# Optimization experiments

Measured on AMD Instinct MI355X. Metric: run time of the kernel, lower is better.

The kernel has to match this reference:

```python
import jax, jax.numpy as jnp
import numpy as np

E, B, C, M, H = 8, 2, 1024, 2048, 7168


def setup_inputs() -> dict:
    key = jax.random.key(0)
    k1, k2, k3, k4 = jax.random.split(key, 4)
    # kaiming_uniform-ish scale for weights (bound = sqrt(6/fan_in)/sqrt(1+5) ~ 1/sqrt(fan_in))
    s_in = 1.0 / np.sqrt(M)
    s_ffn = 1.0 / np.sqrt(H)
    return {
        "dispatch_input": jax.random.normal(k1, (E, B, C, M), dtype=jnp.float32),
        "w1": jax.random.uniform(k2, (E, M, H), dtype=jnp.float32, minval=-s_in, maxval=s_in),
        "w2": jax.random.uniform(k3, (E, H, M), dtype=jnp.float32, minval=-s_ffn, maxval=s_ffn),
        "w3": jax.random.uniform(k4, (E, M, H), dtype=jnp.float32, minval=-s_in, maxval=s_in),
    }


def reference(dispatch_input, w1, w2, w3):
    # Batched per-expert SwiGLU MLP.
    # gate: [E,B,C,H], up: [E,B,C,H]
    gate = jnp.einsum("ebcm,emh->ebch", dispatch_input, w1)
    up = jnp.einsum("ebcm,emh->ebch", dispatch_input, w3)
    hidden = jax.nn.silu(gate) * up
    out = jnp.einsum("ebch,ehm->ebcm", hidden, w2)
    return out
```

## Files before the change

### kernel.cpp

```cpp
#include <hip/hip_runtime.h>

typedef __attribute__((ext_vector_type(8))) short bf16x8;
typedef __attribute__((ext_vector_type(4))) float f32x4;
typedef __attribute__((ext_vector_type(4))) unsigned int u32x4;
typedef __attribute__((ext_vector_type(4))) unsigned short u16x4;

#define NE 8
#define NT 2048
#define NM 2048
#define NH 7168

#define BAR() asm volatile("s_barrier" ::: "memory")
#define WAITV(N) asm volatile("s_waitcnt vmcnt(" #N ")" ::: "memory")

__device__ __forceinline__ unsigned short f2bf(float f) {
    unsigned int u = __float_as_uint(f);
    return (unsigned short)((u + 0x7fffu + ((u >> 16) & 1u)) >> 16);
}

__device__ __forceinline__ void gld16(const void* g, void* l) {
    __builtin_amdgcn_global_load_lds(
        (const __attribute__((address_space(1))) void*)g,
        (__attribute__((address_space(3))) void*)l, 16, 0, 0);
}


__global__ __launch_bounds__(256) void convert_x_kernel(
        const float* __restrict__ in, unsigned short* __restrict__ out) {
    const int i = blockIdx.x * 256 + threadIdx.x;
    f32x4 a = ((const f32x4*)in)[i];
    ((u16x4*)out)[i] = (u16x4){f2bf(a[0]), f2bf(a[1]), f2bf(a[2]), f2bf(a[3])};
}

__global__ __launch_bounds__(256) void convert_wT_kernel(
        const float* __restrict__ in, unsigned short* __restrict__ out,
        int R, int C) {
    const int t = threadIdx.x;
    const int e = blockIdx.y;
    const int tiles_c = C >> 6;
    const int tr = blockIdx.x / tiles_c, tc = blockIdx.x % tiles_c;

    const float* ip = in + (size_t)e * R * C + (size_t)(tr * 64) * C + tc * 64;
    unsigned short* op = out + (size_t)e * R * C + (size_t)(tc * 64) * R + tr * 64;

    __shared__ unsigned short tl[64][68];

    const int rr = t >> 4, c4 = (t & 15) * 4;
#pragma unroll
    for (int q = 0; q < 4; ++q) {
        const int r = q * 16 + rr;
        f32x4 v = *(const f32x4*)(ip + (size_t)r * C + c4);
        *(u16x4*)&tl[r][c4] = (u16x4){f2bf(v[0]), f2bf(v[1]), f2bf(v[2]), f2bf(v[3])};
    }
    __syncthreads();
#pragma unroll
    for (int q = 0; q < 4; ++q) {
        const int oc = q * 16 + rr;
        u16x4 v = (u16x4){tl[c4][oc], tl[c4 + 1][oc], tl[c4 + 2][oc], tl[c4 + 3][oc]};
        *(u16x4*)(op + (size_t)oc * R + c4) = v;
    }
}

__global__ __launch_bounds__(256) void convert_w13_kernel(
        const float* __restrict__ w1, const float* __restrict__ w3,
        unsigned short* __restrict__ wcat) {
    const int t = threadIdx.x;
    const int e = blockIdx.y;
    const int tiles_c = NH >> 6;
    const int tr = blockIdx.x / tiles_c, tc = blockIdx.x % tiles_c;

    __shared__ unsigned short tl[64][68];
    const int rr = t >> 4, c4 = (t & 15) * 4;
    unsigned short* ob = wcat + (size_t)e * (2 * NH) * NM + (size_t)(tc * 128) * NM + tr * 64;

#pragma unroll
    for (int pass = 0; pass < 2; ++pass) {
        const float* ip = (pass ? w3 : w1) + (size_t)e * NM * NH + (size_t)(tr * 64) * NH + tc * 64;
        if (pass) __syncthreads();
#pragma unroll
        for (int q = 0; q < 4; ++q) {
            const int r = q * 16 + rr;
            f32x4 v = *(const f32x4*)(ip + (size_t)r * NH + c4);
            *(u16x4*)&tl[r][c4] = (u16x4){f2bf(v[0]), f2bf(v[1]), f2bf(v[2]), f2bf(v[3])};
        }
        __syncthreads();
#pragma unroll
        for (int q = 0; q < 4; ++q) {
            const int oc = q * 16 + rr;
            const int orow = ((oc >> 4) * 32) + pass * 16 + (oc & 15);
            u16x4 v = (u16x4){tl[c4][oc], tl[c4 + 1][oc], tl[c4 + 2][oc], tl[c4 + 3][oc]};
            *(u16x4*)(ob + (size_t)orow * NM + c4) = v;
        }
    }
}

__global__ __launch_bounds__(512, 2) void gemm1p_kernel(
        const unsigned short* __restrict__ xb, const unsigned short* __restrict__ wcat,
        unsigned short* __restrict__ hid) {
    const int tid = threadIdx.x;
    const int lane = tid & 63, wv = tid >> 6;
    const int wr = wv >> 2, wc = wv & 3;
    const int e = blockIdx.y;
    const int d = blockIdx.x;
    const int l = (d & 7) * 56 + (d >> 3);
    const int ct = l >> 3, tt = l & 7;

    const unsigned short* ag = xb   + (size_t)(e * NT + tt * 256) * NM;
    const unsigned short* bg = wcat + (size_t)e * (2 * NH) * NM + (size_t)(ct * 256) * NM;
    unsigned short* hg = hid + (size_t)(e * NT + tt * 256) * NH + ct * 128;

    __shared__ __align__(16) unsigned short lds[3 * 16384];

    const int frow = lane & 15;
    const int fks  = (lane >> 4) * 8;
    const int la   = lane * 8;
    const int lr   = lane & 15, lq = lane >> 4;

    f32x4 acc[8][4];
#pragma unroll
    for (int m = 0; m < 8; ++m)
#pragma unroll
        for (int n = 0; n < 4; ++n) acc[m][n] = (f32x4){0.f, 0.f, 0.f, 0.f};

    auto stageA = [&](int t, int buf) {
        unsigned short* dst = lds + buf * 16384 + wv * 512;
        const unsigned short* src = ag + (size_t)(wv * 16 + frow) * NM + t * 32 + fks;
        gld16(src, dst);
        gld16(src + (size_t)128 * NM, dst + 8 * 512);
    };
    auto stageB = [&](int t, int buf) {
        unsigned short* dst = lds + buf * 16384 + 8192 + wv * 512;
        const unsigned short* src = bg + (size_t)(wv * 16 + frow) * NM + t * 32 + fks;
        gld16(src, dst);
        gld16(src + (size_t)128 * NM, dst + 8 * 512);
    };

    auto body = [&](int t, int buf, bool st2, int nbuf) {
        const unsigned short* bA = lds + buf * 16384;
        const unsigned short* bB = bA + 8192;
        bf16x8 af[4], bf[4];
        BAR();
#pragma unroll
        for (int m = 0; m < 4; ++m)
            af[m] = *(const bf16x8*)(bA + (wr * 8 + m) * 512 + la);
#pragma unroll
        for (int n = 0; n < 4; ++n)
            bf[n] = *(const bf16x8*)(bB + (wc * 4 + n) * 512 + la);
        __builtin_amdgcn_s_setprio(1);
#pragma unroll
        for (int m = 0; m < 4; ++m)
#pragma unroll
            for (int n = 0; n < 4; ++n)
                acc[m][n] = __builtin_amdgcn_mfma_f32_16x16x32_bf16(af[m], bf[n], acc[m][n], 0, 0, 0);
        __builtin_amdgcn_s_setprio(0);
        if (st2) stageB(t + 2, nbuf);
#pragma unroll
        for (int m = 0; m < 4; ++m)
            af[m] = *(const bf16x8*)(bA + (wr * 8 + 4 + m) * 512 + la);
        __builtin_amdgcn_s_setprio(1);
#pragma unroll
        for (int m = 0; m < 4; ++m)
#pragma unroll
            for (int n = 0; n < 4; ++n)
                acc[4 + m][n] = __builtin_amdgcn_mfma_f32_16x16x32_bf16(af[m], bf[n], acc[4 + m][n], 0, 0, 0);
        __builtin_amdgcn_s_setprio(0);
        BAR();
    };

    const int NKT = NM / 32;
    stageA(0, 0); stageB(0, 0);
    stageA(1, 1); stageB(1, 1);

    int buf = 0, nbuf = 2;
    for (int t = 0; t < NKT - 2; ++t) {
        stageA(t + 2, nbuf);
        WAITV(6);
        body(t, buf, true, nbuf);
        buf = (buf == 2) ? 0 : buf + 1;
        nbuf = (nbuf == 2) ? 0 : nbuf + 1;
    }
    WAITV(4);
    body(NKT - 2, buf, false, 0);
    buf = (buf == 2) ? 0 : buf + 1;
    WAITV(0);
    body(NKT - 1, buf, false, 0);

#pragma unroll
    for (int mf = 0; mf < 8; ++mf)
#pragma unroll
        for (int p = 0; p < 2; ++p)
#pragma unroll
            for (int i = 0; i < 4; ++i) {
                const float g = acc[mf][2 * p][i];
                const float u = acc[mf][2 * p + 1][i];
                const float s = g / (1.f + __expf(-g));
                const int r = wr * 128 + mf * 16 + lq * 4 + i;
                const int h = wc * 32 + p * 16 + lr;
                hg[(size_t)r * NH + h] = f2bf(s * u);
            }
}

__global__ __launch_bounds__(512, 2) void gemm2p_kernel(
        const unsigned short* __restrict__ hid, const unsigned short* __restrict__ w2t,
        float* __restrict__ out) {
    const int tid = threadIdx.x;
    const int lane = tid & 63, wv = tid >> 6;
    const int wr = wv >> 2, wc = wv & 3;
    const int e = blockIdx.y;
    const int d = blockIdx.x;
    const int l = (d & 7) * 8 + (d >> 3);
    const int mt = l >> 3, tt = l & 7;

    const unsigned short* ag = hid + (size_t)(e * NT + tt * 256) * NH;
    const unsigned short* bg = w2t + (size_t)e * NM * NH + (size_t)(mt * 256) * NH;
    float* og = out + (size_t)(e * NT + tt * 256) * NM + mt * 256;

    __shared__ __align__(16) unsigned short lds[3 * 16384];

    const int frow = lane & 15;
    const int fks  = (lane >> 4) * 8;
    const int la   = lane * 8;
    const int lr   = lane & 15, lq = lane >> 4;

    f32x4 acc[8][4];
#pragma unroll
    for (int m = 0; m < 8; ++m)
#pragma unroll
        for (int n = 0; n < 4; ++n) acc[m][n] = (f32x4){0.f, 0.f, 0.f, 0.f};

    auto stageA = [&](int t, int buf) {
        unsigned short* dst = lds + buf * 16384 + wv * 512;
        const unsigned short* src = ag + (size_t)(wv * 16 + frow) * NH + t * 32 + fks;
        gld16(src, dst);
        gld16(src + (size_t)128 * NH, dst + 8 * 512);
    };
    auto stageB = [&](int t, int buf) {
        unsigned short* dst = lds + buf * 16384 + 8192 + wv * 512;
        const unsigned short* src = bg + (size_t)(wv * 16 + frow) * NH + t * 32 + fks;
        gld16(src, dst);
        gld16(src + (size_t)128 * NH, dst + 8 * 512);
    };

    auto body = [&](int t, int buf, bool st2, int nbuf) {
        const unsigned short* bA = lds + buf * 16384;
        const unsigned short* bB = bA + 8192;
        bf16x8 af[4], bf[4];
        BAR();
#pragma unroll
        for (int m = 0; m < 4; ++m)
            af[m] = *(const bf16x8*)(bA + (wr * 8 + m) * 512 + la);
#pragma unroll
        for (int n = 0; n < 4; ++n)
            bf[n] = *(const bf16x8*)(bB + (wc * 4 + n) * 512 + la);
        __builtin_amdgcn_s_setprio(1);
#pragma unroll
        for (int m = 0; m < 4; ++m)
#pragma unroll
            for (int n = 0; n < 4; ++n)
                acc[m][n] = __builtin_amdgcn_mfma_f32_16x16x32_bf16(af[m], bf[n], acc[m][n], 0, 0, 0);
        __builtin_amdgcn_s_setprio(0);
        if (st2) stageB(t + 2, nbuf);
#pragma unroll
        for (int m = 0; m < 4; ++m)
            af[m] = *(const bf16x8*)(bA + (wr * 8 + 4 + m) * 512 + la);
        __builtin_amdgcn_s_setprio(1);
#pragma unroll
        for (int m = 0; m < 4; ++m)
#pragma unroll
            for (int n = 0; n < 4; ++n)
                acc[4 + m][n] = __builtin_amdgcn_mfma_f32_16x16x32_bf16(af[m], bf[n], acc[4 + m][n], 0, 0, 0);
        __builtin_amdgcn_s_setprio(0);
        BAR();
    };

    const int NKT = NH / 32;
    stageA(0, 0); stageB(0, 0);
    stageA(1, 1); stageB(1, 1);

    int buf = 0, nbuf = 2;
    for (int t = 0; t < NKT - 2; ++t) {
        stageA(t + 2, nbuf);
        WAITV(6);
        body(t, buf, true, nbuf);
        buf = (buf == 2) ? 0 : buf + 1;
        nbuf = (nbuf == 2) ? 0 : nbuf + 1;
    }
    WAITV(4);
    body(NKT - 2, buf, false, 0);
    buf = (buf == 2) ? 0 : buf + 1;
    WAITV(0);
    body(NKT - 1, buf, false, 0);

#pragma unroll
    for (int mf = 0; mf < 8; ++mf)
#pragma unroll
        for (int n = 0; n < 4; ++n)
#pragma unroll
            for (int i = 0; i < 4; ++i) {
                const int r = wr * 128 + mf * 16 + lq * 4 + i;
                const int c = wc * 64 + n * 16 + lr;
                og[(size_t)r * NM + c] = acc[mf][n][i];
            }
}

#define ROWB 80
#define TILEB (128 * ROWB)

__global__ __launch_bounds__(256, 2) void gemm1_fb_kernel(
        const float* __restrict__ x, const float* __restrict__ w1,
        const float* __restrict__ w3, unsigned short* __restrict__ hid) {
    const int tid = threadIdx.x;
    const int e = blockIdx.y;
    const int d = blockIdx.x;
    const int l = (d & 7) * 112 + (d >> 3);
    const int hn = l >> 4, tm = l & 15;

    const float* xg  = x  + (size_t)(e * NT + tm * 128) * NM;
    const float* w1g = w1 + (size_t)e * NM * NH + hn * 128;
    const float* w3g = w3 + (size_t)e * NM * NH + hn * 128;
    unsigned short* hg = hid + (size_t)(e * NT + tm * 128) * NH + hn * 128;

    __shared__ __align__(16) unsigned char lds[2 * 3 * TILEB];

    const int a_r = tid >> 3, a_c4 = tid & 7;
    const int w_kq = (tid >> 2) & 7;
    const int w_cg = ((tid >> 5) << 2) | (tid & 3);

    const int lane = tid & 63;
    const int wv = tid >> 6;
    const int r0w = (wv >> 1) * 64, c0w = (wv & 1) * 64;
    const int lr = lane & 15, lq = lane >> 4;

    f32x4 accg[4][4], accu[4][4];
#pragma unroll
    for (int m = 0; m < 4; ++m)
#pragma unroll
        for (int n = 0; n < 4; ++n) {
            accg[m][n] = (f32x4){0.f, 0.f, 0.f, 0.f};
            accu[m][n] = (f32x4){0.f, 0.f, 0.f, 0.f};
        }

    f32x4 la0, la1, la2, la3;
    f32x4 l10, l11, l12, l13, l30, l31, l32, l33;

    auto stage_load = [&](int ks) {
        const int k0 = ks * 32;
        const float* pa = xg + (size_t)a_r * NM + k0 + a_c4 * 4;
        la0 = *(const f32x4*)(pa);
        la1 = *(const f32x4*)(pa + 32 * NM);
        la2 = *(const f32x4*)(pa + 64 * NM);
        la3 = *(const f32x4*)(pa + 96 * NM);
        const float* p1 = w1g + (size_t)(k0 + w_kq * 4) * NH + w_cg * 4;
        l10 = *(const f32x4*)(p1);
        l11 = *(const f32x4*)(p1 + NH);
        l12 = *(const f32x4*)(p1 + 2 * NH);
        l13 = *(const f32x4*)(p1 + 3 * NH);
        const float* p3 = w3g + (size_t)(k0 + w_kq * 4) * NH + w_cg * 4;
        l30 = *(const f32x4*)(p3);
        l31 = *(const f32x4*)(p3 + NH);
        l32 = *(const f32x4*)(p3 + 2 * NH);
        l33 = *(const f32x4*)(p3 + 3 * NH);
    };

    auto stage_write = [&](int buf) {
        unsigned char* base = lds + buf * (3 * TILEB);
        unsigned char* pa = base + a_r * ROWB + a_c4 * 8;
        *(u16x4*)(pa)             = (u16x4){f2bf(la0[0]), f2bf(la0[1]), f2bf(la0[2]), f2bf(la0[3])};
        *(u16x4*)(pa + 32 * ROWB) = (u16x4){f2bf(la1[0]), f2bf(la1[1]), f2bf(la1[2]), f2bf(la1[3])};
        *(u16x4*)(pa + 64 * ROWB) = (u16x4){f2bf(la2[0]), f2bf(la2[1]), f2bf(la2[2]), f2bf(la2[3])};
        *(u16x4*)(pa + 96 * ROWB) = (u16x4){f2bf(la3[0]), f2bf(la3[1]), f2bf(la3[2]), f2bf(la3[3])};
        unsigned char* pw1 = base + TILEB + w_kq * 8;
#pragma unroll
        for (int j = 0; j < 4; ++j) {
            const int c = w_cg * 4 + j;
            *(u16x4*)(pw1 + c * ROWB) =
                (u16x4){f2bf(l10[j]), f2bf(l11[j]), f2bf(l12[j]), f2bf(l13[j])};
        }
        unsigned char* pw3 = base + 2 * TILEB + w_kq * 8;
#pragma unroll
        for (int j = 0; j < 4; ++j) {
            const int c = w_cg * 4 + j;
            *(u16x4*)(pw3 + c * ROWB) =
                (u16x4){f2bf(l30[j]), f2bf(l31[j]), f2bf(l32[j]), f2bf(l33[j])};
        }
    };

    auto compute = [&](int buf) {
        const unsigned char* base = lds + buf * (3 * TILEB);
        bf16x8 af[4], b1f[4], b3f[4];
#pragma unroll
        for (int m = 0; m < 4; ++m)
            af[m] = *(const bf16x8*)(base + (r0w + m * 16 + lr) * ROWB + lq * 16);
#pragma unroll
        for (int n = 0; n < 4; ++n) {
            b1f[n] = *(const bf16x8*)(base + TILEB + (c0w + n * 16 + lr) * ROWB + lq * 16);
            b3f[n] = *(const bf16x8*)(base + 2 * TILEB + (c0w + n * 16 + lr) * ROWB + lq * 16);
        }
#pragma unroll
        for (int m = 0; m < 4; ++m)
#pragma unroll
            for (int n = 0; n < 4; ++n) {
                accg[m][n] = __builtin_amdgcn_mfma_f32_16x16x32_bf16(af[m], b1f[n], accg[m][n], 0, 0, 0);
                accu[m][n] = __builtin_amdgcn_mfma_f32_16x16x32_bf16(af[m], b3f[n], accu[m][n], 0, 0, 0);
            }
    };

    stage_load(0);
    stage_write(0);
    __syncthreads();
    int cur = 0;
    const int NK = NM / 32;
    for (int ks = 0; ks < NK; ++ks) {
        const bool more = (ks + 1 < NK);
        if (more) stage_load(ks + 1);
        compute(cur);
        if (more) {
            stage_write(cur ^ 1);
            __syncthreads();
        }
        cur ^= 1;
    }

#pragma unroll
    for (int m = 0; m < 4; ++m)
#pragma unroll
        for (int n = 0; n < 4; ++n)
#pragma unroll
            for (int i = 0; i < 4; ++i) {
                const float g = accg[m][n][i];
                const float u = accu[m][n][i];
                const float s = g / (1.f + __expf(-g));
                const int r = r0w + m * 16 + lq * 4 + i;
                const int c = c0w + n * 16 + lr;
                hg[(size_t)r * NH + c] = f2bf(s * u);
            }
}

__global__ __launch_bounds__(256, 2) void gemm2_fb_kernel(
        const unsigned short* __restrict__ hid, const float* __restrict__ w2,
        float* __restrict__ out) {
    const int tid = threadIdx.x;
    const int e = blockIdx.y;
    const int d = blockIdx.x;
    const int l = (d & 7) * 32 + (d >> 3);
    const int mn = l >> 4, tm = l & 15;

    const unsigned short* ag = hid + (size_t)(e * NT + tm * 128) * NH;
    const float* wg = w2 + (size_t)e * NH * NM + mn * 128;
    float* og = out + (size_t)(e * NT + tm * 128) * NM + mn * 128;

    __shared__ __align__(16) unsigned char lds[2 * 2 * TILEB];

    const int a_row = tid >> 2, a_ch = tid & 3;
    const int w_kq = (tid >> 2) & 7;
    const int w_cg = ((tid >> 5) << 2) | (tid & 3);

    const int lane = tid & 63;
    const int wv = tid >> 6;
    const int r0w = (wv >> 1) * 64, c0w = (wv & 1) * 64;
    const int lr = lane & 15, lq = lane >> 4;

    f32x4 acc[4][4];
#pragma unroll
    for (int m = 0; m < 4; ++m)
#pragma unroll
        for (int n = 0; n < 4; ++n) acc[m][n] = (f32x4){0.f, 0.f, 0.f, 0.f};

    u32x4 lau0, lau1;
    f32x4 lw0, lw1, lw2, lw3;

    auto stage_load = [&](int ks) {
        const int k0 = ks * 32;
        lau0 = *(const u32x4*)(ag + (size_t)a_row * NH + k0 + a_ch * 8);
        lau1 = *(const u32x4*)(ag + (size_t)(a_row + 64) * NH + k0 + a_ch * 8);
        const float* p = wg + (size_t)(k0 + w_kq * 4) * NM + w_cg * 4;
        lw0 = *(const f32x4*)(p);
        lw1 = *(const f32x4*)(p + NM);
        lw2 = *(const f32x4*)(p + 2 * NM);
        lw3 = *(const f32x4*)(p + 3 * NM);
    };

    auto stage_write = [&](int buf) {
        unsigned char* base = lds + buf * (2 * TILEB);
        *(u32x4*)(base + a_row * ROWB + a_ch * 16) = lau0;
        *(u32x4*)(base + (a_row + 64) * ROWB + a_ch * 16) = lau1;
        unsigned char* pw = base + TILEB + w_kq * 8;
#pragma unroll
        for (int j = 0; j < 4; ++j) {
            const int c = w_cg * 4 + j;
            *(u16x4*)(pw + c * ROWB) =
                (u16x4){f2bf(lw0[j]), f2bf(lw1[j]), f2bf(lw2[j]), f2bf(lw3[j])};
        }
    };

    auto compute = [&](int buf) {
        const unsigned char* base = lds + buf * (2 * TILEB);
        bf16x8 af[4], bf[4];
#pragma unroll
        for (int m = 0; m < 4; ++m)
            af[m] = *(const bf16x8*)(base + (r0w + m * 16 + lr) * ROWB + lq * 16);
#pragma unroll
        for (int n = 0; n < 4; ++n)
            bf[n] = *(const bf16x8*)(base + TILEB + (c0w + n * 16 + lr) * ROWB + lq * 16);
#pragma unroll
        for (int m = 0; m < 4; ++m)
#pragma unroll
            for (int n = 0; n < 4; ++n)
                acc[m][n] = __builtin_amdgcn_mfma_f32_16x16x32_bf16(af[m], bf[n], acc[m][n], 0, 0, 0);
    };

    stage_load(0);
    stage_write(0);
    __syncthreads();
    int cur = 0;
    const int NK = NH / 32;
    for (int ks = 0; ks < NK; ++ks) {
        const bool more = (ks + 1 < NK);
        if (more) stage_load(ks + 1);
        compute(cur);
        if (more) {
            stage_write(cur ^ 1);
            __syncthreads();
        }
        cur ^= 1;
    }

#pragma unroll
    for (int m = 0; m < 4; ++m)
#pragma unroll
        for (int n = 0; n < 4; ++n)
#pragma unroll
            for (int i = 0; i < 4; ++i) {
                const int r = r0w + m * 16 + lq * 4 + i;
                const int c = c0w + n * 16 + lr;
                og[(size_t)r * NM + c] = acc[m][n][i];
            }
}


extern "C" void kernel_launch(void* const* d_in, const int* in_sizes, int n_in,
                              void* d_out, int out_size, void* d_ws, size_t ws_size,
                              hipStream_t stream) {
    const float* x  = (const float*)d_in[0];
    const float* w1 = (const float*)d_in[1];
    const float* w2 = (const float*)d_in[2];
    const float* w3 = (const float*)d_in[3];
    float* out = (float*)d_out;

    const size_t XB_SZ   = (size_t)NE * NT * NM * 2;
    const size_t WCAT_SZ = (size_t)NE * 2 * NH * NM * 2;
    const size_t HID_SZ  = (size_t)NE * NT * NH * 2;
    const size_t NEED = XB_SZ + WCAT_SZ + HID_SZ;

    if (ws_size >= NEED) {
        unsigned char* ws = (unsigned char*)d_ws;
        unsigned short* xbp  = (unsigned short*)(ws);
        unsigned short* wcat = (unsigned short*)(ws + XB_SZ);
        unsigned short* hidb = (unsigned short*)(ws + XB_SZ + WCAT_SZ);
        unsigned short* w2t  = (unsigned short*)(ws);

        convert_x_kernel<<<dim3((NE * NT * NM) / 1024), 256, 0, stream>>>(x, xbp);
        convert_w13_kernel<<<dim3((NM / 64) * (NH / 64), NE), 256, 0, stream>>>(w1, w3, wcat);
        gemm1p_kernel<<<dim3(448, NE), 512, 0, stream>>>(xbp, wcat, hidb);
        convert_wT_kernel<<<dim3((NH / 64) * (NM / 64), NE), 256, 0, stream>>>(w2, w2t, NH, NM);
        gemm2p_kernel<<<dim3(64, NE), 512, 0, stream>>>(hidb, w2t, out);
    } else {
        unsigned short* hid = (unsigned short*)d_ws;
        gemm1_fb_kernel<<<dim3(896, NE), 256, 0, stream>>>(x, w1, w3, hid);
        gemm2_fb_kernel<<<dim3(256, NE), 256, 0, stream>>>(hid, w2, out);
    }
}
```

Before: 1.937 ms.

## Load B fragments directly from global into registers, drop B LDS staging

Both bf16 GEMM kernels stop staging the B (weight) tile through LDS. Each wave now loads its B fragments straight from global memory into registers, double-buffered across two register sets, while A keeps its triple-buffered LDS pipeline. LDS use is halved and the B ds_reads go away. In exchange B loads lose sharing across the waves in a block (wr=0/1 waves fetch the same B), which raises global/L2 traffic. It also depends on hand-tuned vmcnt waits staying correct.

```diff
diff --git a/kernel.cpp b/kernel.cpp
--- a/kernel.cpp
+++ b/kernel.cpp
@@ -109,7 +109,7 @@
     const unsigned short* bg = wcat + (size_t)e * (2 * NH) * NM + (size_t)(ct * 256) * NM;
     unsigned short* hg = hid + (size_t)(e * NT + tt * 256) * NH + ct * 128;
 
-    __shared__ __align__(16) unsigned short lds[3 * 16384];
+    __shared__ __align__(16) unsigned short lds[3 * 8192];
 
     const int frow = lane & 15;
     const int fks  = (lane >> 4) * 8;
@@ -123,29 +123,23 @@
         for (int n = 0; n < 4; ++n) acc[m][n] = (f32x4){0.f, 0.f, 0.f, 0.f};
 
     auto stageA = [&](int t, int buf) {
-        unsigned short* dst = lds + buf * 16384 + wv * 512;
+        unsigned short* dst = lds + buf * 8192 + wv * 512;
         const unsigned short* src = ag + (size_t)(wv * 16 + frow) * NM + t * 32 + fks;
         gld16(src, dst);
         gld16(src + (size_t)128 * NM, dst + 8 * 512);
     };
-    auto stageB = [&](int t, int buf) {
-        unsigned short* dst = lds + buf * 16384 + 8192 + wv * 512;
-        const unsigned short* src = bg + (size_t)(wv * 16 + frow) * NM + t * 32 + fks;
-        gld16(src, dst);
-        gld16(src + (size_t)128 * NM, dst + 8 * 512);
-    };
-
-    auto body = [&](int t, int buf, bool st2, int nbuf) {
-        const unsigned short* bA = lds + buf * 16384;
-        const unsigned short* bB = bA + 8192;
-        bf16x8 af[4], bf[4];
-        BAR();
+    auto bload = [&](bf16x8 (&bf)[4], int t) {
+#pragma unroll
+        for (int n = 0; n < 4; ++n)
+            bf[n] = *(const bf16x8*)(bg + (size_t)(wc * 64 + n * 16 + lr) * NM + t * 32 + fks);
+    };
+
+    auto body = [&](int buf, const bf16x8 (&bf)[4]) {
+        const unsigned short* bA = lds + buf * 8192;
+        bf16x8 af[4];
 #pragma unroll
         for (int m = 0; m < 4; ++m)
             af[m] = *(const bf16x8*)(bA + (wr * 8 + m) * 512 + la);
-#pragma unroll
-        for (int n = 0; n < 4; ++n)
-            bf[n] = *(const bf16x8*)(bB + (wc * 4 + n) * 512 + la);
         __builtin_amdgcn_s_setprio(1);
 #pragma unroll
         for (int m = 0; m < 4; ++m)
@@ -153,7 +147,6 @@
             for (int n = 0; n < 4; ++n)
                 acc[m][n] = __builtin_amdgcn_mfma_f32_16x16x32_bf16(af[m], bf[n], acc[m][n], 0, 0, 0);
         __builtin_amdgcn_s_setprio(0);
-        if (st2) stageB(t + 2, nbuf);
 #pragma unroll
         for (int m = 0; m < 4; ++m)
             af[m] = *(const bf16x8*)(bA + (wr * 8 + 4 + m) * 512 + la);
@@ -164,26 +157,40 @@
             for (int n = 0; n < 4; ++n)
                 acc[4 + m][n] = __builtin_amdgcn_mfma_f32_16x16x32_bf16(af[m], bf[n], acc[4 + m][n], 0, 0, 0);
         __builtin_amdgcn_s_setprio(0);
+    };
+
+    const int NKT = NM / 32;
+    bf16x8 bfA[4], bfB[4];
+
+    stageA(0, 0);
+    bload(bfA, 0);
+    stageA(1, 1);
+
+    int buf = 0, nbuf = 2;
+    for (int t = 0; t < NKT - 2; t += 2) {
+        bload(bfB, t + 1);
+        stageA(t + 2, nbuf);
+        WAITV(12); BAR(); WAITV(8);
+        body(buf, bfA);
         BAR();
-    };
-
-    const int NKT = NM / 32;
-    stageA(0, 0); stageB(0, 0);
-    stageA(1, 1); stageB(1, 1);
-
-    int buf = 0, nbuf = 2;
-    for (int t = 0; t < NKT - 2; ++t) {
-        stageA(t + 2, nbuf);
-        WAITV(6);
-        body(t, buf, true, nbuf);
         buf = (buf == 2) ? 0 : buf + 1;
         nbuf = (nbuf == 2) ? 0 : nbuf + 1;
-    }
-    WAITV(4);
-    body(NKT - 2, buf, false, 0);
+
+        bload(bfA, t + 2);
+        stageA(t + 3, nbuf);
+        WAITV(12); BAR(); WAITV(8);
+        body(buf, bfB);
+        BAR();
+        buf = (buf == 2) ? 0 : buf + 1;
+        nbuf = (nbuf == 2) ? 0 : nbuf + 1;
+    }
+    bload(bfB, NKT - 1);
+    WAITV(10); BAR(); WAITV(6);
+    body(buf, bfA);
+    BAR();
     buf = (buf == 2) ? 0 : buf + 1;
-    WAITV(0);
-    body(NKT - 1, buf, false, 0);
+    WAITV(4); BAR(); WAITV(0);
+    body(buf, bfB);
 
 #pragma unroll
     for (int mf = 0; mf < 8; ++mf)
@@ -215,7 +222,7 @@
     const unsigned short* bg = w2t + (size_t)e * NM * NH + (size_t)(mt * 256) * NH;
     float* og = out + (size_t)(e * NT + tt * 256) * NM + mt * 256;
 
-    __shared__ __align__(16) unsigned short lds[3 * 16384];
+    __shared__ __align__(16) unsigned short lds[3 * 8192];
 
     const int frow = lane & 15;
     const int fks  = (lane >> 4) * 8;
@@ -229,29 +236,23 @@
         for (int n = 0; n < 4; ++n) acc[m][n] = (f32x4){0.f, 0.f, 0.f, 0.f};
 
     auto stageA = [&](int t, int buf) {
-        unsigned short* dst = lds + buf * 16384 + wv * 512;
+        unsigned short* dst = lds + buf * 8192 + wv * 512;
         const unsigned short* src = ag + (size_t)(wv * 16 + frow) * NH + t * 32 + fks;
         gld16(src, dst);
         gld16(src + (size_t)128 * NH, dst + 8 * 512);
     };
-    auto stageB = [&](int t, int buf) {
-        unsigned short* dst = lds + buf * 16384 + 8192 + wv * 512;
-        const unsigned short* src = bg + (size_t)(wv * 16 + frow) * NH + t * 32 + fks;
-        gld16(src, dst);
-        gld16(src + (size_t)128 * NH, dst + 8 * 512);
-    };
-
-    auto body = [&](int t, int buf, bool st2, int nbuf) {
-        const unsigned short* bA = lds + buf * 16384;
-        const unsigned short* bB = bA + 8192;
-        bf16x8 af[4], bf[4];
-        BAR();
+    auto bload = [&](bf16x8 (&bf)[4], int t) {
+#pragma unroll
+        for (int n = 0; n < 4; ++n)
+            bf[n] = *(const bf16x8*)(bg + (size_t)(wc * 64 + n * 16 + lr) * NH + t * 32 + fks);
+    };
+
+    auto body = [&](int buf, const bf16x8 (&bf)[4]) {
+        const unsigned short* bA = lds + buf * 8192;
+        bf16x8 af[4];
 #pragma unroll
         for (int m = 0; m < 4; ++m)
             af[m] = *(const bf16x8*)(bA + (wr * 8 + m) * 512 + la);
-#pragma unroll
-        for (int n = 0; n < 4; ++n)
-            bf[n] = *(const bf16x8*)(bB + (wc * 4 + n) * 512 + la);
         __builtin_amdgcn_s_setprio(1);
 #pragma unroll
         for (int m = 0; m < 4; ++m)
@@ -259,7 +260,6 @@
             for (int n = 0; n < 4; ++n)
                 acc[m][n] = __builtin_amdgcn_mfma_f32_16x16x32_bf16(af[m], bf[n], acc[m][n], 0, 0, 0);
         __builtin_amdgcn_s_setprio(0);
-        if (st2) stageB(t + 2, nbuf);
 #pragma unroll
         for (int m = 0; m < 4; ++m)
             af[m] = *(const bf16x8*)(bA + (wr * 8 + 4 + m) * 512 + la);
@@ -270,26 +270,40 @@
             for (int n = 0; n < 4; ++n)
                 acc[4 + m][n] = __builtin_amdgcn_mfma_f32_16x16x32_bf16(af[m], bf[n], acc[4 + m][n], 0, 0, 0);
         __builtin_amdgcn_s_setprio(0);
+    };
+
+    const int NKT = NH / 32;
+    bf16x8 bfA[4], bfB[4];
+
+    stageA(0, 0);
+    bload(bfA, 0);
+    stageA(1, 1);
+
+    int buf = 0, nbuf = 2;
+    for (int t = 0; t < NKT - 2; t += 2) {
+        bload(bfB, t + 1);
+        stageA(t + 2, nbuf);
+        WAITV(12); BAR(); WAITV(8);
+        body(buf, bfA);
         BAR();
-    };
-
-    const int NKT = NH / 32;
-    stageA(0, 0); stageB(0, 0);
-    stageA(1, 1); stageB(1, 1);
-
-    int buf = 0, nbuf = 2;
-    for (int t = 0; t < NKT - 2; ++t) {
-        stageA(t + 2, nbuf);
-        WAITV(6);
-        body(t, buf, true, nbuf);
         buf = (buf == 2) ? 0 : buf + 1;
         nbuf = (nbuf == 2) ? 0 : nbuf + 1;
-    }
-    WAITV(4);
-    body(NKT - 2, buf, false, 0);
+
+        bload(bfA, t + 2);
+        stageA(t + 3, nbuf);
+        WAITV(12); BAR(); WAITV(8);
+        body(buf, bfB);
+        BAR();
+        buf = (buf == 2) ? 0 : buf + 1;
+        nbuf = (nbuf == 2) ? 0 : nbuf + 1;
+    }
+    bload(bfB, NKT - 1);
+    WAITV(10); BAR(); WAITV(6);
+    body(buf, bfA);
+    BAR();
     buf = (buf == 2) ? 0 : buf + 1;
-    WAITV(0);
-    body(NKT - 1, buf, false, 0);
+    WAITV(4); BAR(); WAITV(0);
+    body(buf, bfB);
 
 #pragma unroll
     for (int mf = 0; mf < 8; ++mf)
```

Result: slower. 2.896 ms (+49.5%).

## Replace triple-buffered LDS pipeline with simple double buffering in both GEMMs

Applied to the files above, without the earlier changes.

Both bf16 GEMM kernels drop from a three-stage LDS ring with prefetch distance two, where the B load was interleaved mid-body, to two buffers with prefetch distance one. A and B for the next tile are issued together before the barrier. LDS use per block shrinks from 96KB to 64KB, which may ease occupancy pressure. The cost is less latency hiding for global loads and a simpler schedule that no longer splits the B stage between the MFMA halves.

```diff
diff --git a/kernel.cpp b/kernel.cpp
--- a/kernel.cpp
+++ b/kernel.cpp
@@ -109,7 +109,7 @@
     const unsigned short* bg = wcat + (size_t)e * (2 * NH) * NM + (size_t)(ct * 256) * NM;
     unsigned short* hg = hid + (size_t)(e * NT + tt * 256) * NH + ct * 128;
 
-    __shared__ __align__(16) unsigned short lds[3 * 16384];
+    __shared__ __align__(16) unsigned short lds[2 * 16384];
 
     const int frow = lane & 15;
     const int fks  = (lane >> 4) * 8;
@@ -135,11 +135,10 @@
         gld16(src + (size_t)128 * NM, dst + 8 * 512);
     };
 
-    auto body = [&](int t, int buf, bool st2, int nbuf) {
+    auto body = [&](int buf) {
         const unsigned short* bA = lds + buf * 16384;
         const unsigned short* bB = bA + 8192;
         bf16x8 af[4], bf[4];
-        BAR();
 #pragma unroll
         for (int m = 0; m < 4; ++m)
             af[m] = *(const bf16x8*)(bA + (wr * 8 + m) * 512 + la);
@@ -153,7 +152,6 @@
             for (int n = 0; n < 4; ++n)
                 acc[m][n] = __builtin_amdgcn_mfma_f32_16x16x32_bf16(af[m], bf[n], acc[m][n], 0, 0, 0);
         __builtin_amdgcn_s_setprio(0);
-        if (st2) stageB(t + 2, nbuf);
 #pragma unroll
         for (int m = 0; m < 4; ++m)
             af[m] = *(const bf16x8*)(bA + (wr * 8 + 4 + m) * 512 + la);
@@ -164,26 +162,25 @@
             for (int n = 0; n < 4; ++n)
                 acc[4 + m][n] = __builtin_amdgcn_mfma_f32_16x16x32_bf16(af[m], bf[n], acc[4 + m][n], 0, 0, 0);
         __builtin_amdgcn_s_setprio(0);
-        BAR();
     };
 
     const int NKT = NM / 32;
     stageA(0, 0); stageB(0, 0);
-    stageA(1, 1); stageB(1, 1);
-
-    int buf = 0, nbuf = 2;
-    for (int t = 0; t < NKT - 2; ++t) {
-        stageA(t + 2, nbuf);
-        WAITV(6);
-        body(t, buf, true, nbuf);
-        buf = (buf == 2) ? 0 : buf + 1;
-        nbuf = (nbuf == 2) ? 0 : nbuf + 1;
-    }
-    WAITV(4);
-    body(NKT - 2, buf, false, 0);
-    buf = (buf == 2) ? 0 : buf + 1;
-    WAITV(0);
-    body(NKT - 1, buf, false, 0);
+
+    int buf = 0;
+    for (int t = 0; t < NKT; ++t) {
+        if (t + 1 < NKT) {
+            stageA(t + 1, buf ^ 1);
+            stageB(t + 1, buf ^ 1);
+            WAITV(4);
+        } else {
+            WAITV(0);
+        }
+        BAR();
+        body(buf);
+        BAR();
+        buf ^= 1;
+    }
 
 #pragma unroll
     for (int mf = 0; mf < 8; ++mf)
@@ -215,7 +212,7 @@
     const unsigned short* bg = w2t + (size_t)e * NM * NH + (size_t)(mt * 256) * NH;
     float* og = out + (size_t)(e * NT + tt * 256) * NM + mt * 256;
 
-    __shared__ __align__(16) unsigned short lds[3 * 16384];
+    __shared__ __align__(16) unsigned short lds[2 * 16384];
 
     const int frow = lane & 15;
     const int fks  = (lane >> 4) * 8;
@@ -241,11 +238,10 @@
         gld16(src + (size_t)128 * NH, dst + 8 * 512);
     };
 
-    auto body = [&](int t, int buf, bool st2, int nbuf) {
+    auto body = [&](int buf) {
         const unsigned short* bA = lds + buf * 16384;
         const unsigned short* bB = bA + 8192;
         bf16x8 af[4], bf[4];
-        BAR();
 #pragma unroll
         for (int m = 0; m < 4; ++m)
             af[m] = *(const bf16x8*)(bA + (wr * 8 + m) * 512 + la);
@@ -259,7 +255,6 @@
             for (int n = 0; n < 4; ++n)
                 acc[m][n] = __builtin_amdgcn_mfma_f32_16x16x32_bf16(af[m], bf[n], acc[m][n], 0, 0, 0);
         __builtin_amdgcn_s_setprio(0);
-        if (st2) stageB(t + 2, nbuf);
 #pragma unroll
         for (int m = 0; m < 4; ++m)
             af[m] = *(const bf16x8*)(bA + (wr * 8 + 4 + m) * 512 + la);
@@ -270,26 +265,25 @@
             for (int n = 0; n < 4; ++n)
                 acc[4 + m][n] = __builtin_amdgcn_mfma_f32_16x16x32_bf16(af[m], bf[n], acc[4 + m][n], 0, 0, 0);
         __builtin_amdgcn_s_setprio(0);
-        BAR();
     };
 
     const int NKT = NH / 32;
     stageA(0, 0); stageB(0, 0);
-    stageA(1, 1); stageB(1, 1);
-
-    int buf = 0, nbuf = 2;
-    for (int t = 0; t < NKT - 2; ++t) {
-        stageA(t + 2, nbuf);
-        WAITV(6);
-        body(t, buf, true, nbuf);
-        buf = (buf == 2) ? 0 : buf + 1;
-        nbuf = (nbuf == 2) ? 0 : nbuf + 1;
-    }
-    WAITV(4);
-    body(NKT - 2, buf, false, 0);
-    buf = (buf == 2) ? 0 : buf + 1;
-    WAITV(0);
-    body(NKT - 1, buf, false, 0);
+
+    int buf = 0;
+    for (int t = 0; t < NKT; ++t) {
+        if (t + 1 < NKT) {
+            stageA(t + 1, buf ^ 1);
+            stageB(t + 1, buf ^ 1);
+            WAITV(4);
+        } else {
+            WAITV(0);
+        }
+        BAR();
+        body(buf);
+        BAR();
+        buf ^= 1;
+    }
 
 #pragma unroll
     for (int mf = 0; mf < 8; ++mf)
```

New measurement: 2.009 ms. 1.04x slower.

## Fold w2 transpose-convert into gemm1 launch as extra blocks

Applied to the files above, without the earlier changes.

Appends 1792 extra blocks to the gemm1 grid that perform the w2 fp32-to-bf16 transpose into a separate workspace region, removing the standalone convert_wT launch. The transpose work can then overlap with the tail of the first GEMM instead of running serially between the GEMMs. It needs extra workspace for w2t; if that is unavailable it falls back to the old path. Block scheduling order may delay GEMM blocks or compete for bandwidth.

```diff
diff --git a/kernel.cpp b/kernel.cpp
--- a/kernel.cpp
+++ b/kernel.cpp
@@ -96,20 +96,47 @@
 
 __global__ __launch_bounds__(512, 2) void gemm1p_kernel(
         const unsigned short* __restrict__ xb, const unsigned short* __restrict__ wcat,
-        unsigned short* __restrict__ hid) {
+        unsigned short* __restrict__ hid,
+        const float* __restrict__ w2, unsigned short* __restrict__ w2t) {
     const int tid = threadIdx.x;
+    const int e = blockIdx.y;
+    const int d = blockIdx.x;
+
+    __shared__ __align__(16) unsigned short lds[3 * 16384];
+
+    if (d >= 448) {
+        const int t = tid & 255;
+        const int tile = (d - 448) * 2 + (tid >> 8);
+        const int tr = tile >> 5, tc = tile & 31;
+        const float* ip = w2 + (size_t)e * NH * NM + (size_t)(tr * 64) * NM + tc * 64;
+        unsigned short* op = w2t + (size_t)e * NM * NH + (size_t)(tc * 64) * NH + tr * 64;
+        unsigned short (*tl)[68] = (unsigned short (*)[68])(lds + (tid >> 8) * 4352);
+
+        const int rr = t >> 4, c4 = (t & 15) * 4;
+#pragma unroll
+        for (int q = 0; q < 4; ++q) {
+            const int r = q * 16 + rr;
+            f32x4 v = *(const f32x4*)(ip + (size_t)r * NM + c4);
+            *(u16x4*)&tl[r][c4] = (u16x4){f2bf(v[0]), f2bf(v[1]), f2bf(v[2]), f2bf(v[3])};
+        }
+        __syncthreads();
+#pragma unroll
+        for (int q = 0; q < 4; ++q) {
+            const int oc = q * 16 + rr;
+            u16x4 v = (u16x4){tl[c4][oc], tl[c4 + 1][oc], tl[c4 + 2][oc], tl[c4 + 3][oc]};
+            *(u16x4*)(op + (size_t)oc * NH + c4) = v;
+        }
+        return;
+    }
+
     const int lane = tid & 63, wv = tid >> 6;
     const int wr = wv >> 2, wc = wv & 3;
-    const int e = blockIdx.y;
-    const int d = blockIdx.x;
     const int l = (d & 7) * 56 + (d >> 3);
     const int ct = l >> 3, tt = l & 7;
 
     const unsigned short* ag = xb   + (size_t)(e * NT + tt * 256) * NM;
     const unsigned short* bg = wcat + (size_t)e * (2 * NH) * NM + (size_t)(ct * 256) * NM;
     unsigned short* hg = hid + (size_t)(e * NT + tt * 256) * NH + ct * 128;
-
-    __shared__ __align__(16) unsigned short lds[3 * 16384];
 
     const int frow = lane & 15;
     const int fks  = (lane >> 4) * 8;
@@ -550,10 +577,23 @@
     const size_t XB_SZ   = (size_t)NE * NT * NM * 2;
     const size_t WCAT_SZ = (size_t)NE * 2 * NH * NM * 2;
     const size_t HID_SZ  = (size_t)NE * NT * NH * 2;
-    const size_t NEED = XB_SZ + WCAT_SZ + HID_SZ;
-
-    if (ws_size >= NEED) {
-        unsigned char* ws = (unsigned char*)d_ws;
+    const size_t W2T_SZ  = (size_t)NE * NM * NH * 2;
+    const size_t NEED_FULL = XB_SZ + WCAT_SZ + HID_SZ + W2T_SZ;
+    const size_t NEED_STD  = XB_SZ + WCAT_SZ + HID_SZ;
+
+    unsigned char* ws = (unsigned char*)d_ws;
+
+    if (ws_size >= NEED_FULL) {
+        unsigned short* xbp  = (unsigned short*)(ws);
+        unsigned short* wcat = (unsigned short*)(ws + XB_SZ);
+        unsigned short* hidb = (unsigned short*)(ws + XB_SZ + WCAT_SZ);
+        unsigned short* w2t  = (unsigned short*)(ws + XB_SZ + WCAT_SZ + HID_SZ);
+
+        convert_x_kernel<<<dim3((NE * NT * NM) / 1024), 256, 0, stream>>>(x, xbp);
+        convert_w13_kernel<<<dim3((NM / 64) * (NH / 64), NE), 256, 0, stream>>>(w1, w3, wcat);
+        gemm1p_kernel<<<dim3(448 + 1792, NE), 512, 0, stream>>>(xbp, wcat, hidb, w2, w2t);
+        gemm2p_kernel<<<dim3(64, NE), 512, 0, stream>>>(hidb, w2t, out);
+    } else if (ws_size >= NEED_STD) {
         unsigned short* xbp  = (unsigned short*)(ws);
         unsigned short* wcat = (unsigned short*)(ws + XB_SZ);
         unsigned short* hidb = (unsigned short*)(ws + XB_SZ + WCAT_SZ);
@@ -561,7 +601,7 @@
 
         convert_x_kernel<<<dim3((NE * NT * NM) / 1024), 256, 0, stream>>>(x, xbp);
         convert_w13_kernel<<<dim3((NM / 64) * (NH / 64), NE), 256, 0, stream>>>(w1, w3, wcat);
-        gemm1p_kernel<<<dim3(448, NE), 512, 0, stream>>>(xbp, wcat, hidb);
+        gemm1p_kernel<<<dim3(448, NE), 512, 0, stream>>>(xbp, wcat, hidb, w2, w2t);
         convert_wT_kernel<<<dim3((NH / 64) * (NM / 64), NE), 256, 0, stream>>>(w2, w2t, NH, NM);
         gemm2p_kernel<<<dim3(64, NE), 512, 0, stream>>>(hidb, w2t, out);
     } else {
```

After: 1.932 ms. No clear change (-0.3%).
